# Kernel tuning notes

Hardware: AMD Instinct MI355X
Metric: run time of the kernel (lower is better)

The kernel has to match this reference:

```python
import jax, jax.numpy as jnp
import numpy as np

N, K, H, X_DIM, S_DIM = 50000, 8, 128, 32, 27
LSTM_IN = X_DIM + 3 * H  # 416


def setup_inputs() -> dict:
    key = jax.random.key(0)
    ks = jax.random.split(key, 16)

    def u(k, shape, fan_in):
        lim = 1.0 / np.sqrt(fan_in)
        return jax.random.uniform(k, shape, jnp.float32, -lim, lim)

    return {
        "x": jax.random.normal(ks[0], (N, X_DIM), jnp.float32),
        "h_self": jax.random.normal(ks[1], (N, H), jnp.float32),
        "c_self": jax.random.normal(ks[2], (N, H), jnp.float32),
        "h_inflows": jax.random.normal(ks[3], (N, K, H), jnp.float32),
        "inflow_valid": jax.random.randint(ks[4], (N, K), 0, 2) > 0,
        "static": jax.random.normal(ks[5], (N, S_DIM), jnp.float32),
        # Linear weights stored (out, in) as in eqx.nn.Linear
        "Wn": u(ks[6], (H, H), H),                     # W_neighbor, no bias
        "Wg": u(ks[7], (H, 2 * H), 2 * H),             # W_inflow_gate
        "bg": u(ks[8], (H,), 2 * H),
        "Ws": u(ks[9], (H, S_DIM), S_DIM),             # W_static
        "bs": u(ks[10], (H,), S_DIM),
        "Wl": u(ks[11], (4 * H, LSTM_IN), LSTM_IN),    # W_lstm
        "bl": u(ks[12], (4 * H,), LSTM_IN),
        "ln_w": jnp.ones((H,), jnp.float32),           # ln_h affine
        "ln_b": jnp.zeros((H,), jnp.float32),
    }


def reference(x, h_self, c_self, h_inflows, inflow_valid, static,
              Wn, Wg, bg, Ws, bs, Wl, bl, ln_w, ln_b):
    eps = 1e-5
    # per-neighbor message: [N,K,H]
    msgs = jnp.einsum('nkh,oh->nko', h_inflows, Wn)
    # inflow gate on concat(h_inflow, h_self): [N,K,H]
    h_tiled = jnp.broadcast_to(h_self[:, None, :], h_inflows.shape)
    gate_in = jnp.concatenate([h_inflows, h_tiled], axis=-1)  # [N,K,2H]
    gates = jax.nn.sigmoid(jnp.einsum('nkd,od->nko', gate_in, Wg) + bg)
    # masked sum over neighbors -> [N,H]
    mask = inflow_valid[..., None].astype(jnp.float32)
    neighbor_context = jnp.sum(gates * msgs * mask, axis=1)
    static_proj = static @ Ws.T + bs  # [N,H]
    combined = jnp.concatenate([x, h_self, neighbor_context, static_proj], axis=-1)
    z = combined @ Wl.T + bl  # [N,4H]
    i, f, o, g = jnp.split(z, 4, axis=-1)
    c_new = jax.nn.sigmoid(f) * c_self + jax.nn.sigmoid(i) * jnp.tanh(g)
    h_new = jax.nn.sigmoid(o) * jnp.tanh(c_new)
    # LayerNorm over hidden dim (eqx default eps=1e-5, affine)
    mu = jnp.mean(h_new, axis=-1, keepdims=True)
    var = jnp.mean(jnp.square(h_new - mu), axis=-1, keepdims=True)
    h_new = (h_new - mu) * jax.lax.rsqrt(var + eps) * ln_w + ln_b
    return (h_new, c_new)
```

## Files before the change

### kernel.cpp

```cpp
#include <hip/hip_runtime.h>
#include <hip/hip_bf16.h>

#define NN 50000
#define KI 8
#define H 128
#define XD 32
#define SD 27
#define CIN 416
#define CIN2 320
#define CPAD 328
#define ZOUT 512
#define NTILE_NB (NN / KI)
#define MB_LSTM 32

typedef __attribute__((ext_vector_type(8))) short bf16x8;
typedef __attribute__((ext_vector_type(4))) float f32x4;
typedef __attribute__((ext_vector_type(4))) unsigned short us4;

#define MFMA16(a, b, c) __builtin_amdgcn_mfma_f32_16x16x32_bf16((a), (b), (c), 0, 0, 0)

static __device__ __forceinline__ float sigmoidf_(float x) {
    return 1.0f / (1.0f + __expf(-x));
}
static __device__ __forceinline__ float tanhf_(float x) {
    return 1.0f - 2.0f / (__expf(2.0f * x) + 1.0f);
}
static __device__ __forceinline__ unsigned short bf(float f) {
    __hip_bfloat16 h = __float2bfloat16(f);
    return __builtin_bit_cast(unsigned short, h);
}
static __device__ __forceinline__ float dot4_(float4 a, float4 b) {
    return a.x * b.x + a.y * b.y + a.z * b.z + a.w * b.w;
}

__global__ __launch_bounds__(256) void k_prep(
    const float* __restrict__ Wn, const float* __restrict__ Wg,
    const float* __restrict__ Wl, const float* __restrict__ bl,
    const float* __restrict__ Ws, const float* __restrict__ bs,
    unsigned short* __restrict__ WnB, unsigned short* __restrict__ WgB,
    unsigned short* __restrict__ WpB, float* __restrict__ bp)
{
    const int b = blockIdx.x, t = threadIdx.x;
    if (b < 512) {
        const float* wr = Wl + (size_t)b * CIN;
        unsigned short* out = WpB + (size_t)b * CIN2;
        for (int c = t; c < CIN2; c += 256) {
            float v;
            if (c < 288) v = wr[c];
            else if (c < 288 + SD) {
                int s = c - 288;
                float acc = 0.f;
                for (int j = 0; j < H; ++j) acc += wr[288 + j] * Ws[j * SD + s];
                v = acc;
            } else v = 0.f;
            out[c] = bf(v);
        }
        if (t == 0) {
            float acc = bl[b];
            for (int j = 0; j < H; ++j) acc += wr[288 + j] * bs[j];
            bp[b] = acc;
        }
    } else {
        int idx = (b - 512) * 256 + t;
        for (int r = idx; r < 49152; r += 16384) {
            if (r < 16384) WnB[r] = bf(Wn[r]);
            else WgB[r - 16384] = bf(Wg[r - 16384]);
        }
    }
}

__global__ __launch_bounds__(256, 2) void k_nb_mfma(
    const float* __restrict__ hself_g, const float* __restrict__ hin_g,
    const unsigned char* __restrict__ valid_raw,
    const unsigned short* __restrict__ WnB, const unsigned short* __restrict__ WgB,
    const float* __restrict__ bg,
    unsigned short* __restrict__ ncb, int nc_stride)
{
    __shared__ unsigned short hin_s[64 * 128];
    __shared__ unsigned short hs_s[8 * 128];
    __shared__ float gh_s[8][128];
    __shared__ unsigned short ncs[8 * 128];
    __shared__ float valid_s[64];

    const int t = threadIdx.x;
    const int w = t >> 6, l = t & 63;
    const int ln = l & 15, lk = l >> 4;

    int det = 0;
    #pragma unroll
    for (int i = 0; i < 64; ++i) det |= valid_raw[4 * i + 1];
    const bool f8 = (det != 0);

    bf16x8 Bn[2][4], Ba[2][4], Bb[2][4];
    const int cbase = w * 32;
    #pragma unroll
    for (int c = 0; c < 2; ++c) {
        const int col = cbase + c * 16 + ln;
        #pragma unroll
        for (int kk = 0; kk < 4; ++kk) {
            const int k0 = kk * 32 + lk * 8;
            Bn[c][kk] = *(const bf16x8*)(WnB + col * H + k0);
            Ba[c][kk] = *(const bf16x8*)(WgB + col * 2 * H + k0);
            Bb[c][kk] = *(const bf16x8*)(WgB + col * 2 * H + H + k0);
        }
    }
    const float bg0 = bg[cbase + ln];
    const float bg1 = bg[cbase + 16 + ln];

    float4 ph[8], ps;
    float pv = 0.f;
    {
        const int nb0 = blockIdx.x * 8;
        const float4* src = (const float4*)(hin_g + (size_t)nb0 * KI * H);
        #pragma unroll
        for (int i = 0; i < 8; ++i) ph[i] = src[t + i * 256];
        ps = ((const float4*)(hself_g + (size_t)nb0 * H))[t];
        if (t < 64)
            pv = (f8 ? (valid_raw[(size_t)nb0 * KI + t] != 0)
                     : (((const unsigned int*)valid_raw)[(size_t)nb0 * KI + t] != 0u))
                     ? 1.f : 0.f;
    }

    for (int tile = blockIdx.x; tile < NTILE_NB; tile += gridDim.x) {
        const int nb = tile * 8;

        if (t < 64) valid_s[t] = pv;
        #pragma unroll
        for (int i = 0; i < 8; ++i) {
            int e = (t + i * 256) * 4, row = e >> 7, col = e & 127;
            unsigned byte = (unsigned)(row * 256 + col * 2) ^ (unsigned)((row & 7) << 4);
            us4 pk = { bf(ph[i].x), bf(ph[i].y), bf(ph[i].z), bf(ph[i].w) };
            *(us4*)((char*)hin_s + byte) = pk;
        }
        {
            int e = t * 4, row = e >> 7, col = e & 127;
            unsigned byte = (unsigned)(row * 256 + col * 2) ^ (unsigned)((row & 7) << 4);
            us4 pk = { bf(ps.x), bf(ps.y), bf(ps.z), bf(ps.w) };
            *(us4*)((char*)hs_s + byte) = pk;
        }
        __syncthreads();

        const int next = tile + gridDim.x;
        if (next < NTILE_NB) {
            const int nb2 = next * 8;
            const float4* src = (const float4*)(hin_g + (size_t)nb2 * KI * H);
            #pragma unroll
            for (int i = 0; i < 8; ++i) ph[i] = src[t + i * 256];
            ps = ((const float4*)(hself_g + (size_t)nb2 * H))[t];
            if (t < 64)
                pv = (f8 ? (valid_raw[(size_t)nb2 * KI + t] != 0)
                         : (((const unsigned int*)valid_raw)[(size_t)nb2 * KI + t] != 0u))
                         ? 1.f : 0.f;
        }

        f32x4 accM[4][2], accP[4][2], accG[2];
        #pragma unroll
        for (int m = 0; m < 4; ++m)
            #pragma unroll
            for (int c = 0; c < 2; ++c) { accM[m][c] = (f32x4)0.f; accP[m][c] = (f32x4)0.f; }
        accG[0] = (f32x4)0.f; accG[1] = (f32x4)0.f;

        #pragma unroll
        for (int kk = 0; kk < 4; ++kk) {
            const int k0 = kk * 32 + lk * 8;
            bf16x8 am[4];
            #pragma unroll
            for (int m = 0; m < 4; ++m) {
                int row = m * 16 + ln;
                unsigned byte = (unsigned)(row * 256 + k0 * 2) ^ (unsigned)((row & 7) << 4);
                am[m] = *(const bf16x8*)((const char*)hin_s + byte);
            }
            bf16x8 ah;
            {
                int row = ln & 7;
                unsigned byte = (unsigned)(row * 256 + k0 * 2) ^ (unsigned)((row & 7) << 4);
                ah = *(const bf16x8*)((const char*)hs_s + byte);
            }
            #pragma unroll
            for (int m = 0; m < 4; ++m)
                #pragma unroll
                for (int c = 0; c < 2; ++c) {
                    accM[m][c] = MFMA16(am[m], Bn[c][kk], accM[m][c]);
                    accP[m][c] = MFMA16(am[m], Ba[c][kk], accP[m][c]);
                }
            accG[0] = MFMA16(ah, Bb[0][kk], accG[0]);
            accG[1] = MFMA16(ah, Bb[1][kk], accG[1]);
        }

        #pragma unroll
        for (int c = 0; c < 2; ++c)
            #pragma unroll
            for (int r = 0; r < 4; ++r) {
                int row = lk * 4 + r;
                if (row < 8) gh_s[row][cbase + c * 16 + ln] = accG[c][r];
            }
        __syncthreads();

        #pragma unroll
        for (int m = 0; m < 4; ++m) {
            const int node = 2 * m + (lk >> 1);
            #pragma unroll
            for (int c = 0; c < 2; ++c) {
                const int col = cbase + c * 16 + ln;
                const float bgc = c ? bg1 : bg0;
                const float ghv = gh_s[node][col];
                float sum = 0.f;
                #pragma unroll
                for (int r = 0; r < 4; ++r) {
                    int row = m * 16 + lk * 4 + r;
                    float g = sigmoidf_(accP[m][c][r] + ghv + bgc);
                    sum += valid_s[row] * g * accM[m][c][r];
                }
                sum += __shfl_xor(sum, 16);
                if ((l & 16) == 0) ncs[(2 * m + (l >> 5)) * H + col] = bf(sum);
            }
        }
        __syncthreads();

        {
            int e = t * 4, node = e >> 7, col = e & 127;
            us4 v = *(const us4*)(ncs + e);
            *(us4*)(ncb + (size_t)(nb + node) * nc_stride + col) = v;
        }
    }
}

__global__ __launch_bounds__(512, 4) void k_lstm_mfma(
    const float* __restrict__ x_g, const float* __restrict__ hself_g,
    const float* __restrict__ cself_g, const float* __restrict__ stat_g,
    const unsigned short* __restrict__ ncb, int nc_stride,
    const unsigned short* __restrict__ WpB, const float* __restrict__ bp,
    const float* __restrict__ lnw, const float* __restrict__ lnb,
    float* __restrict__ h_out, float* __restrict__ c_out)
{
    __shared__ char smem[MB_LSTM * CPAD * 2];
    unsigned short* comb = (unsigned short*)smem;
    float (*hpre)[132] = (float(*)[132])smem;

    const int t = threadIdx.x;
    const int nb = blockIdx.x * MB_LSTM;
    const int w = t >> 6, l = t & 63, ln = l & 15, lk = l >> 4;
    const int hcol = w * 16 + ln;

    if (t < 256) {
        int e = t * 4, row = e >> 5, col = e & 31;
        us4 pk = { 0, 0, 0, 0 };
        if (nb + row < NN) {
            float4 v = ((const float4*)(x_g + (size_t)nb * XD))[t];
            pk = us4{ bf(v.x), bf(v.y), bf(v.z), bf(v.w) };
        }
        *(us4*)(comb + row * CPAD + col) = pk;
    }
    #pragma unroll
    for (int i = 0; i < 2; ++i) {
        int p4 = t + i * 512;
        int e = p4 * 4, row = e >> 7, col = 32 + (e & 127);
        us4 pk = { 0, 0, 0, 0 };
        if (nb + row < NN) {
            float4 v = ((const float4*)(hself_g + (size_t)nb * H))[p4];
            pk = us4{ bf(v.x), bf(v.y), bf(v.z), bf(v.w) };
        }
        *(us4*)(comb + row * CPAD + col) = pk;
    }
    #pragma unroll
    for (int i = 0; i < 2; ++i) {
        int p4 = t + i * 512;
        int e = p4 * 4, row = e >> 7, col = e & 127;
        us4 v = { 0, 0, 0, 0 };
        if (nb + row < NN) v = *(const us4*)(ncb + (size_t)(nb + row) * nc_stride + col);
        *(us4*)(comb + row * CPAD + 160 + col) = v;
    }
    for (int i = t; i < MB_LSTM * SD; i += 512) {
        int row = i / SD, col = i - row * SD;
        unsigned short v = 0;
        if (nb + row < NN) v = bf(stat_g[(size_t)(nb + row) * SD + col]);
        comb[row * CPAD + 288 + col] = v;
    }
    if (t < MB_LSTM * 5) {
        int row = t / 5, col = 315 + t % 5;
        comb[row * CPAD + col] = 0;
    }

    float cpre[8];
    #pragma unroll
    for (int m = 0; m < 2; ++m)
        #pragma unroll
        for (int r = 0; r < 4; ++r) {
            int node = m * 16 + lk * 4 + r;
            size_t n = (size_t)(nb + node);
            cpre[m * 4 + r] = (n < NN) ? cself_g[n * H + hcol] : 0.f;
        }
    __syncthreads();

    f32x4 acc[2][4];
    #pragma unroll
    for (int m = 0; m < 2; ++m)
        #pragma unroll
        for (int g = 0; g < 4; ++g) acc[m][g] = (f32x4)0.f;

    #pragma unroll
    for (int kk = 0; kk < 10; ++kk) {
        const int k0 = kk * 32 + lk * 8;
        bf16x8 a0 = *(const bf16x8*)(comb + ln * CPAD + k0);
        bf16x8 a1 = *(const bf16x8*)(comb + (16 + ln) * CPAD + k0);
        #pragma unroll
        for (int g = 0; g < 4; ++g) {
            bf16x8 b = *(const bf16x8*)(WpB + (size_t)(g * H + hcol) * CIN2 + k0);
            acc[0][g] = MFMA16(a0, b, acc[0][g]);
            acc[1][g] = MFMA16(a1, b, acc[1][g]);
        }
    }
    __syncthreads();

    {
        const float bi = bp[hcol], bff = bp[H + hcol];
        const float bo = bp[2 * H + hcol], bgg = bp[3 * H + hcol];
        #pragma unroll
        for (int m = 0; m < 2; ++m)
            #pragma unroll
            for (int r = 0; r < 4; ++r) {
                int node = m * 16 + lk * 4 + r;
                size_t n = (size_t)(nb + node);
                if (n < NN) {
                    float zi = acc[m][0][r] + bi;
                    float zf = acc[m][1][r] + bff;
                    float zo = acc[m][2][r] + bo;
                    float zg = acc[m][3][r] + bgg;
                    float cn = sigmoidf_(zf) * cpre[m * 4 + r] + sigmoidf_(zi) * tanhf_(zg);
                    c_out[n * H + hcol] = cn;
                    hpre[node][hcol] = sigmoidf_(zo) * tanhf_(cn);
                }
            }
    }
    __syncthreads();

    #pragma unroll
    for (int jj = 0; jj < 4; ++jj) {
        const int j = w * 4 + jj;
        const size_t n = (size_t)(nb + j);
        if (n < NN) {
            float a = hpre[j][l];
            float b = hpre[j][64 + l];
            float s = a + b, q = a * a + b * b;
            #pragma unroll
            for (int off = 1; off < 64; off <<= 1) {
                s += __shfl_xor(s, off);
                q += __shfl_xor(q, off);
            }
            float mu = s * (1.0f / 128.0f);
            float var = q * (1.0f / 128.0f) - mu * mu;
            float rstd = rsqrtf(var + 1e-5f);
            h_out[n * H + l]      = (a - mu) * rstd * lnw[l] + lnb[l];
            h_out[n * H + 64 + l] = (b - mu) * rstd * lnw[64 + l] + lnb[64 + l];
        }
    }
}

__global__ __launch_bounds__(256) void k_nb_f32(
    const float* __restrict__ hself_g, const float* __restrict__ hin_g,
    const unsigned char* __restrict__ valid_raw,
    const float* __restrict__ Wn, const float* __restrict__ Wg,
    const float* __restrict__ bg, float* __restrict__ nc)
{
    __shared__ float4 hin_s[8 * KI * (H / 4)];
    __shared__ float4 hs_s[8 * (H / 4)];
    __shared__ int flag8;
    const int t = threadIdx.x;
    const int nb = blockIdx.x * 8;
    {
        int loc = 0;
        if (t < 64) {
            #pragma unroll
            for (int i = 0; i < 16; ++i) loc |= valid_raw[4 * (t * 16 + i) + 1];
        }
        int any = __any(loc != 0);
        if (t == 0) flag8 = any;
    }
    const float4* src_hin = (const float4*)(hin_g + (size_t)nb * KI * H);
    #pragma unroll
    for (int i = 0; i < 8; ++i) hin_s[t + i * 256] = src_hin[t + i * 256];
    hs_s[t] = ((const float4*)(hself_g + (size_t)nb * H))[t];
    __syncthreads();
    const int o = t & 127, g = t >> 7;
    float msg[4][KI], gat[4][KI], gh[4];
    #pragma unroll
    for (int j = 0; j < 4; ++j) {
        gh[j] = 0.f;
        #pragma unroll
        for (int k = 0; k < KI; ++k) { msg[j][k] = 0.f; gat[j][k] = 0.f; }
    }
    const float4* Wn4 = (const float4*)(Wn + (size_t)o * H);
    const float4* Wg4a = (const float4*)(Wg + (size_t)o * 2 * H);
    const float4* Wg4b = (const float4*)(Wg + (size_t)o * 2 * H + H);
    for (int d4 = 0; d4 < H / 4; ++d4) {
        float4 wn = Wn4[d4], w0 = Wg4a[d4], w1 = Wg4b[d4];
        #pragma unroll
        for (int j = 0; j < 4; ++j) {
            const int node = g * 4 + j;
            gh[j] += dot4_(w1, hs_s[node * 32 + d4]);
            #pragma unroll
            for (int k = 0; k < KI; ++k) {
                float4 hv = hin_s[(node * KI + k) * 32 + d4];
                msg[j][k] += dot4_(wn, hv);
                gat[j][k] += dot4_(w0, hv);
            }
        }
    }
    const float bgo = bg[o];
    const unsigned int* valid32 = (const unsigned int*)valid_raw;
    const int f8 = flag8;
    #pragma unroll
    for (int j = 0; j < 4; ++j) {
        const int n = nb + g * 4 + j;
        float acc = 0.f;
        #pragma unroll
        for (int k = 0; k < KI; ++k) {
            bool v = f8 ? (valid_raw[n * KI + k] != 0) : (valid32[n * KI + k] != 0u);
            if (v) acc += sigmoidf_(gat[j][k] + gh[j] + bgo) * msg[j][k];
        }
        nc[(size_t)n * H + o] = acc;
    }
}

__global__ __launch_bounds__(256) void k_lstm_f32(
    const float* __restrict__ x_g, const float* __restrict__ hself_g,
    const float* __restrict__ cself_g, const float* __restrict__ stat_g,
    const float* __restrict__ nc,
    const float* __restrict__ Ws, const float* __restrict__ bs,
    const float* __restrict__ Wl, const float* __restrict__ bl,
    const float* __restrict__ lnw, const float* __restrict__ lnb,
    float* __restrict__ h_out, float* __restrict__ c_out)
{
    __shared__ float4 comb4[16 * (CIN / 4)];
    __shared__ float zsh[16 * ZOUT];
    __shared__ float stat_s[16 * SD];
    float* combf = (float*)comb4;
    const int t = threadIdx.x;
    const int nb = blockIdx.x * 16;
    #pragma unroll
    for (int i = 0; i < 2; ++i) {
        int idx = t + i * 256;
        combf[(idx >> 5) * CIN + (idx & 31)] = x_g[(size_t)nb * XD + idx];
    }
    #pragma unroll
    for (int i = 0; i < 8; ++i) {
        int idx = t + i * 256;
        combf[(idx >> 7) * CIN + 32 + (idx & 127)] = hself_g[(size_t)nb * H + idx];
    }
    #pragma unroll
    for (int i = 0; i < 8; ++i) {
        int idx = t + i * 256;
        combf[(idx >> 7) * CIN + 160 + (idx & 127)] = nc[(size_t)nb * H + idx];
    }
    stat_s[t] = stat_g[(size_t)nb * SD + t];
    if (t < 16 * SD - 256) stat_s[t + 256] = stat_g[(size_t)nb * SD + t + 256];
    __syncthreads();
    {
        const int o = t & 127, jg = t >> 7;
        #pragma unroll
        for (int jj = 0; jj < 8; ++jj) {
            const int j = jg * 8 + jj;
            float s = bs[o];
            #pragma unroll
            for (int c = 0; c < SD; ++c) s += Ws[o * SD + c] * stat_s[j * SD + c];
            combf[j * CIN + 288 + o] = s;
        }
    }
    __syncthreads();
    float acc0[16], acc1[16];
    #pragma unroll
    for (int j = 0; j < 16; ++j) { acc0[j] = 0.f; acc1[j] = 0.f; }
    const float4* W0 = (const float4*)(Wl + (size_t)t * CIN);
    const float4* W1 = (const float4*)(Wl + (size_t)(t + 256) * CIN);
    for (int d4 = 0; d4 < CIN / 4; ++d4) {
        float4 w0 = W0[d4], w1 = W1[d4];
        #pragma unroll
        for (int j = 0; j < 16; ++j) {
            float4 cv = comb4[j * (CIN / 4) + d4];
            acc0[j] += dot4_(w0, cv);
            acc1[j] += dot4_(w1, cv);
        }
    }
    const float bl0 = bl[t], bl1 = bl[t + 256];
    #pragma unroll
    for (int j = 0; j < 16; ++j) {
        zsh[j * ZOUT + t] = acc0[j] + bl0;
        zsh[j * ZOUT + 256 + t] = acc1[j] + bl1;
    }
    __syncthreads();
    {
        const int h = t & 127, jg = t >> 7;
        #pragma unroll
        for (int jj = 0; jj < 8; ++jj) {
            const int j = jg * 8 + jj;
            const size_t n = (size_t)(nb + j);
            float zi = zsh[j * ZOUT + h];
            float zf = zsh[j * ZOUT + 128 + h];
            float zo = zsh[j * ZOUT + 256 + h];
            float zg = zsh[j * ZOUT + 384 + h];
            float cn = sigmoidf_(zf) * cself_g[n * H + h] + sigmoidf_(zi) * tanhf(zg);
            c_out[n * H + h] = cn;
            zsh[j * ZOUT + h] = sigmoidf_(zo) * tanhf(cn);
        }
    }
    __syncthreads();
    {
        const int w = t >> 6, lane = t & 63;
        #pragma unroll
        for (int jj = 0; jj < 4; ++jj) {
            const int j = w * 4 + jj;
            const size_t n = (size_t)(nb + j);
            float a = zsh[j * ZOUT + lane];
            float b = zsh[j * ZOUT + 64 + lane];
            float s = a + b, q = a * a + b * b;
            #pragma unroll
            for (int off = 1; off < 64; off <<= 1) {
                s += __shfl_xor(s, off);
                q += __shfl_xor(q, off);
            }
            float mu = s * (1.0f / 128.0f);
            float var = q * (1.0f / 128.0f) - mu * mu;
            float rstd = rsqrtf(var + 1e-5f);
            h_out[n * H + lane] = (a - mu) * rstd * lnw[lane] + lnb[lane];
            h_out[n * H + 64 + lane] = (b - mu) * rstd * lnw[64 + lane] + lnb[64 + lane];
        }
    }
}

extern "C" void kernel_launch(void* const* d_in, const int* in_sizes, int n_in,
                              void* d_out, int out_size, void* d_ws, size_t ws_size,
                              hipStream_t stream) {
    const float* x      = (const float*)d_in[0];
    const float* h_self = (const float*)d_in[1];
    const float* c_self = (const float*)d_in[2];
    const float* h_inf  = (const float*)d_in[3];
    const unsigned char* valid = (const unsigned char*)d_in[4];
    const float* statp  = (const float*)d_in[5];
    const float* Wn     = (const float*)d_in[6];
    const float* Wg     = (const float*)d_in[7];
    const float* bg     = (const float*)d_in[8];
    const float* Ws     = (const float*)d_in[9];
    const float* bs     = (const float*)d_in[10];
    const float* Wl     = (const float*)d_in[11];
    const float* bl     = (const float*)d_in[12];
    const float* lnw    = (const float*)d_in[13];
    const float* lnb    = (const float*)d_in[14];

    float* h_out = (float*)d_out;
    float* c_out = h_out + (size_t)NN * H;

    const size_t W_BYTES = (size_t)512 * CIN2 * 2 + 16384 * 2 + 32768 * 2 + 512 * 4;
    const size_t NC_BYTES = (size_t)NN * H * 2;

    if (ws_size >= W_BYTES) {
        char* p = (char*)d_ws;
        unsigned short* WpB = (unsigned short*)p;           p += (size_t)512 * CIN2 * 2;
        unsigned short* WnB = (unsigned short*)p;           p += 16384 * 2;
        unsigned short* WgB = (unsigned short*)p;           p += 32768 * 2;
        float* bp = (float*)p;                              p += 512 * 4;

        unsigned short* ncb;
        int nc_stride;
        if (ws_size >= W_BYTES + NC_BYTES + 64) {
            ncb = (unsigned short*)p;
            nc_stride = H;
        } else {
            ncb = (unsigned short*)h_out;
            nc_stride = 256;
        }

        k_prep<<<576, 256, 0, stream>>>(Wn, Wg, Wl, bl, Ws, bs,
                                        WnB, WgB, WpB, bp);
        k_nb_mfma<<<512, 256, 0, stream>>>(h_self, h_inf, valid, WnB, WgB, bg,
                                           ncb, nc_stride);
        k_lstm_mfma<<<(NN + MB_LSTM - 1) / MB_LSTM, 512, 0, stream>>>(
            x, h_self, c_self, statp, ncb, nc_stride, WpB, bp,
            lnw, lnb, h_out, c_out);
    } else {
        float* nc_buf = (ws_size >= (size_t)NN * H * sizeof(float))
                            ? (float*)d_ws : h_out;
        k_nb_f32<<<NN / 8, 256, 0, stream>>>(h_self, h_inf, valid, Wn, Wg, bg, nc_buf);
        k_lstm_f32<<<NN / 16, 256, 0, stream>>>(x, h_self, c_self, statp, nc_buf,
                                                Ws, bs, Wl, bl, lnw, lnb, h_out, c_out);
    }
}
```

Baseline: 212.7 us.

## Cut register pressure in neighbor kernel to raise occupancy and grid size

The neighbor-message kernel no longer keeps all Wn/Wg B-fragments in registers or software-prefetches the next tile. Instead it reloads weight fragments from global/L2 inside the k-loop and processes the 64 neighbor rows in two halves, which shrinks the accumulator footprint. Launch bounds rise to 3 blocks per SM and the grid doubles to 1024 blocks, so more waves are resident to hide latency in place of explicit prefetching. The cost is repeated weight loads per tile and losing the register-level overlap of the next tile's global load with compute.

```diff
diff --git a/kernel.cpp b/kernel.cpp
--- a/kernel.cpp
+++ b/kernel.cpp
@@ -12,6 +12,7 @@
 #define ZOUT 512
 #define NTILE_NB (NN / KI)
 #define MB_LSTM 32
+#define GRID_NB 1024
 
 typedef __attribute__((ext_vector_type(8))) short bf16x8;
 typedef __attribute__((ext_vector_type(4))) float f32x4;
@@ -69,7 +70,7 @@
     }
 }
 
-__global__ __launch_bounds__(256, 2) void k_nb_mfma(
+__global__ __launch_bounds__(256, 3) void k_nb_mfma(
     const float* __restrict__ hself_g, const float* __restrict__ hin_g,
     const unsigned char* __restrict__ valid_raw,
     const unsigned short* __restrict__ WnB, const unsigned short* __restrict__ WgB,
@@ -91,100 +92,77 @@
     for (int i = 0; i < 64; ++i) det |= valid_raw[4 * i + 1];
     const bool f8 = (det != 0);
 
-    bf16x8 Bn[2][4], Ba[2][4], Bb[2][4];
     const int cbase = w * 32;
-    #pragma unroll
-    for (int c = 0; c < 2; ++c) {
-        const int col = cbase + c * 16 + ln;
+    const float bg0 = bg[cbase + ln];
+    const float bg1 = bg[cbase + 16 + ln];
+
+    for (int tile = blockIdx.x; tile < NTILE_NB; tile += gridDim.x) {
+        const int nb = tile * 8;
+
+        if (t < 64)
+            valid_s[t] = (f8 ? (valid_raw[(size_t)nb * KI + t] != 0)
+                             : (((const unsigned int*)valid_raw)[(size_t)nb * KI + t] != 0u))
+                             ? 1.f : 0.f;
+        {
+            const float4* src = (const float4*)(hin_g + (size_t)nb * KI * H);
+            float4 r0[8];
+            #pragma unroll
+            for (int i = 0; i < 8; ++i) r0[i] = src[t + i * 256];
+            float4 hv = ((const float4*)(hself_g + (size_t)nb * H))[t];
+            #pragma unroll
+            for (int i = 0; i < 8; ++i) {
+                int e = (t + i * 256) * 4, row = e >> 7, col = e & 127;
+                unsigned byte = (unsigned)(row * 256 + col * 2) ^ (unsigned)((row & 7) << 4);
+                us4 pk = { bf(r0[i].x), bf(r0[i].y), bf(r0[i].z), bf(r0[i].w) };
+                *(us4*)((char*)hin_s + byte) = pk;
+            }
+            {
+                int e = t * 4, row = e >> 7, col = e & 127;
+                unsigned byte = (unsigned)(row * 256 + col * 2) ^ (unsigned)((row & 7) << 4);
+                us4 pk = { bf(hv.x), bf(hv.y), bf(hv.z), bf(hv.w) };
+                *(us4*)((char*)hs_s + byte) = pk;
+            }
+        }
+        __syncthreads();
+
+        f32x4 aM[2][2], aP[2][2], aG[2];
+        #pragma unroll
+        for (int mm = 0; mm < 2; ++mm)
+            #pragma unroll
+            for (int c = 0; c < 2; ++c) { aM[mm][c] = (f32x4)0.f; aP[mm][c] = (f32x4)0.f; }
+        aG[0] = (f32x4)0.f; aG[1] = (f32x4)0.f;
+
         #pragma unroll
         for (int kk = 0; kk < 4; ++kk) {
             const int k0 = kk * 32 + lk * 8;
-            Bn[c][kk] = *(const bf16x8*)(WnB + col * H + k0);
-            Ba[c][kk] = *(const bf16x8*)(WgB + col * 2 * H + k0);
-            Bb[c][kk] = *(const bf16x8*)(WgB + col * 2 * H + H + k0);
-        }
-    }
-    const float bg0 = bg[cbase + ln];
-    const float bg1 = bg[cbase + 16 + ln];
-
-    float4 ph[8], ps;
-    float pv = 0.f;
-    {
-        const int nb0 = blockIdx.x * 8;
-        const float4* src = (const float4*)(hin_g + (size_t)nb0 * KI * H);
-        #pragma unroll
-        for (int i = 0; i < 8; ++i) ph[i] = src[t + i * 256];
-        ps = ((const float4*)(hself_g + (size_t)nb0 * H))[t];
-        if (t < 64)
-            pv = (f8 ? (valid_raw[(size_t)nb0 * KI + t] != 0)
-                     : (((const unsigned int*)valid_raw)[(size_t)nb0 * KI + t] != 0u))
-                     ? 1.f : 0.f;
-    }
-
-    for (int tile = blockIdx.x; tile < NTILE_NB; tile += gridDim.x) {
-        const int nb = tile * 8;
-
-        if (t < 64) valid_s[t] = pv;
-        #pragma unroll
-        for (int i = 0; i < 8; ++i) {
-            int e = (t + i * 256) * 4, row = e >> 7, col = e & 127;
-            unsigned byte = (unsigned)(row * 256 + col * 2) ^ (unsigned)((row & 7) << 4);
-            us4 pk = { bf(ph[i].x), bf(ph[i].y), bf(ph[i].z), bf(ph[i].w) };
-            *(us4*)((char*)hin_s + byte) = pk;
-        }
-        {
-            int e = t * 4, row = e >> 7, col = e & 127;
-            unsigned byte = (unsigned)(row * 256 + col * 2) ^ (unsigned)((row & 7) << 4);
-            us4 pk = { bf(ps.x), bf(ps.y), bf(ps.z), bf(ps.w) };
-            *(us4*)((char*)hs_s + byte) = pk;
-        }
-        __syncthreads();
-
-        const int next = tile + gridDim.x;
-        if (next < NTILE_NB) {
-            const int nb2 = next * 8;
-            const float4* src = (const float4*)(hin_g + (size_t)nb2 * KI * H);
-            #pragma unroll
-            for (int i = 0; i < 8; ++i) ph[i] = src[t + i * 256];
-            ps = ((const float4*)(hself_g + (size_t)nb2 * H))[t];
-            if (t < 64)
-                pv = (f8 ? (valid_raw[(size_t)nb2 * KI + t] != 0)
-                         : (((const unsigned int*)valid_raw)[(size_t)nb2 * KI + t] != 0u))
-                         ? 1.f : 0.f;
-        }
-
-        f32x4 accM[4][2], accP[4][2], accG[2];
-        #pragma unroll
-        for (int m = 0; m < 4; ++m)
-            #pragma unroll
-            for (int c = 0; c < 2; ++c) { accM[m][c] = (f32x4)0.f; accP[m][c] = (f32x4)0.f; }
-        accG[0] = (f32x4)0.f; accG[1] = (f32x4)0.f;
-
-        #pragma unroll
-        for (int kk = 0; kk < 4; ++kk) {
-            const int k0 = kk * 32 + lk * 8;
-            bf16x8 am[4];
-            #pragma unroll
-            for (int m = 0; m < 4; ++m) {
-                int row = m * 16 + ln;
+            bf16x8 am0, am1, ah;
+            {
+                int row = ln;
                 unsigned byte = (unsigned)(row * 256 + k0 * 2) ^ (unsigned)((row & 7) << 4);
-                am[m] = *(const bf16x8*)((const char*)hin_s + byte);
-            }
-            bf16x8 ah;
+                am0 = *(const bf16x8*)((const char*)hin_s + byte);
+            }
+            {
+                int row = 16 + ln;
+                unsigned byte = (unsigned)(row * 256 + k0 * 2) ^ (unsigned)((row & 7) << 4);
+                am1 = *(const bf16x8*)((const char*)hin_s + byte);
+            }
             {
                 int row = ln & 7;
                 unsigned byte = (unsigned)(row * 256 + k0 * 2) ^ (unsigned)((row & 7) << 4);
                 ah = *(const bf16x8*)((const char*)hs_s + byte);
             }
             #pragma unroll
-            for (int m = 0; m < 4; ++m)
-                #pragma unroll
-                for (int c = 0; c < 2; ++c) {
-                    accM[m][c] = MFMA16(am[m], Bn[c][kk], accM[m][c]);
-                    accP[m][c] = MFMA16(am[m], Ba[c][kk], accP[m][c]);
-                }
-            accG[0] = MFMA16(ah, Bb[0][kk], accG[0]);
-            accG[1] = MFMA16(ah, Bb[1][kk], accG[1]);
+            for (int c = 0; c < 2; ++c) {
+                const int col = cbase + c * 16 + ln;
+                bf16x8 bn = *(const bf16x8*)(WnB + col * H + k0);
+                bf16x8 ba = *(const bf16x8*)(WgB + col * 2 * H + k0);
+                bf16x8 bb = *(const bf16x8*)(WgB + col * 2 * H + H + k0);
+                aM[0][c] = MFMA16(am0, bn, aM[0][c]);
+                aM[1][c] = MFMA16(am1, bn, aM[1][c]);
+                aP[0][c] = MFMA16(am0, ba, aP[0][c]);
+                aP[1][c] = MFMA16(am1, ba, aP[1][c]);
+                aG[c]    = MFMA16(ah, bb, aG[c]);
+            }
         }
 
         #pragma unroll
@@ -192,13 +170,13 @@
             #pragma unroll
             for (int r = 0; r < 4; ++r) {
                 int row = lk * 4 + r;
-                if (row < 8) gh_s[row][cbase + c * 16 + ln] = accG[c][r];
+                if (row < 8) gh_s[row][cbase + c * 16 + ln] = aG[c][r];
             }
         __syncthreads();
 
         #pragma unroll
-        for (int m = 0; m < 4; ++m) {
-            const int node = 2 * m + (lk >> 1);
+        for (int mm = 0; mm < 2; ++mm) {
+            const int node = 2 * mm + (lk >> 1);
             #pragma unroll
             for (int c = 0; c < 2; ++c) {
                 const int col = cbase + c * 16 + ln;
@@ -207,12 +185,63 @@
                 float sum = 0.f;
                 #pragma unroll
                 for (int r = 0; r < 4; ++r) {
-                    int row = m * 16 + lk * 4 + r;
-                    float g = sigmoidf_(accP[m][c][r] + ghv + bgc);
-                    sum += valid_s[row] * g * accM[m][c][r];
+                    int row = mm * 16 + lk * 4 + r;
+                    float g = sigmoidf_(aP[mm][c][r] + ghv + bgc);
+                    sum += valid_s[row] * g * aM[mm][c][r];
                 }
                 sum += __shfl_xor(sum, 16);
-                if ((l & 16) == 0) ncs[(2 * m + (l >> 5)) * H + col] = bf(sum);
+                if ((l & 16) == 0) ncs[(2 * mm + (l >> 5)) * H + col] = bf(sum);
+            }
+        }
+
+        #pragma unroll
+        for (int mm = 0; mm < 2; ++mm)
+            #pragma unroll
+            for (int c = 0; c < 2; ++c) { aM[mm][c] = (f32x4)0.f; aP[mm][c] = (f32x4)0.f; }
+
+        #pragma unroll
+        for (int kk = 0; kk < 4; ++kk) {
+            const int k0 = kk * 32 + lk * 8;
+            bf16x8 am0, am1;
+            {
+                int row = 32 + ln;
+                unsigned byte = (unsigned)(row * 256 + k0 * 2) ^ (unsigned)((row & 7) << 4);
+                am0 = *(const bf16x8*)((const char*)hin_s + byte);
+            }
+            {
+                int row = 48 + ln;
+                unsigned byte = (unsigned)(row * 256 + k0 * 2) ^ (unsigned)((row & 7) << 4);
+                am1 = *(const bf16x8*)((const char*)hin_s + byte);
+            }
+            #pragma unroll
+            for (int c = 0; c < 2; ++c) {
+                const int col = cbase + c * 16 + ln;
+                bf16x8 bn = *(const bf16x8*)(WnB + col * H + k0);
+                bf16x8 ba = *(const bf16x8*)(WgB + col * 2 * H + k0);
+                aM[0][c] = MFMA16(am0, bn, aM[0][c]);
+                aM[1][c] = MFMA16(am1, bn, aM[1][c]);
+                aP[0][c] = MFMA16(am0, ba, aP[0][c]);
+                aP[1][c] = MFMA16(am1, ba, aP[1][c]);
+            }
+        }
+
+        #pragma unroll
+        for (int mm = 0; mm < 2; ++mm) {
+            const int node = 4 + 2 * mm + (lk >> 1);
+            #pragma unroll
+            for (int c = 0; c < 2; ++c) {
+                const int col = cbase + c * 16 + ln;
+                const float bgc = c ? bg1 : bg0;
+                const float ghv = gh_s[node][col];
+                float sum = 0.f;
+                #pragma unroll
+                for (int r = 0; r < 4; ++r) {
+                    int row = (2 + mm) * 16 + lk * 4 + r;
+                    float g = sigmoidf_(aP[mm][c][r] + ghv + bgc);
+                    sum += valid_s[row] * g * aM[mm][c][r];
+                }
+                sum += __shfl_xor(sum, 16);
+                if ((l & 16) == 0) ncs[(4 + 2 * mm + (l >> 5)) * H + col] = bf(sum);
             }
         }
         __syncthreads();
@@ -571,8 +600,8 @@
 
         k_prep<<<576, 256, 0, stream>>>(Wn, Wg, Wl, bl, Ws, bs,
                                         WnB, WgB, WpB, bp);
-        k_nb_mfma<<<512, 256, 0, stream>>>(h_self, h_inf, valid, WnB, WgB, bg,
-                                           ncb, nc_stride);
+        k_nb_mfma<<<GRID_NB, 256, 0, stream>>>(h_self, h_inf, valid, WnB, WgB, bg,
+                                               ncb, nc_stride);
         k_lstm_mfma<<<(NN + MB_LSTM - 1) / MB_LSTM, 512, 0, stream>>>(
             x, h_self, c_self, statp, ncb, nc_stride, WpB, bp,
             lnw, lnb, h_out, c_out);
```

After: 247.0 us. +16.1%, slower.

## Stream neighbor tiles via async global-to-LDS double buffering in k_nb_mfma

Applied to the files above, without the earlier changes.

The neighbor kernel now copies raw fp32 h_inflows and h_self tiles straight into LDS with global_load_lds into a double buffer, replacing the register prefetch and bf16 staging. The bf16 conversion moves to the fragment-load step. Weight fragments are reloaded from global/L2 on every k-step instead of being held in registers, which frees VGPRs. The valid mask is read directly into registers, and outputs are written straight to global, dropping two LDS staging buffers and one barrier. The cost is twice the LDS footprint, which may limit occupancy, plus repeated weight reads and conversion work inside the inner loop.

```diff
diff --git a/kernel.cpp b/kernel.cpp
--- a/kernel.cpp
+++ b/kernel.cpp
@@ -12,12 +12,17 @@
 #define ZOUT 512
 #define NTILE_NB (NN / KI)
 #define MB_LSTM 32
+#define GRID_NB 512
 
 typedef __attribute__((ext_vector_type(8))) short bf16x8;
 typedef __attribute__((ext_vector_type(4))) float f32x4;
 typedef __attribute__((ext_vector_type(4))) unsigned short us4;
+typedef __attribute__((ext_vector_type(8))) unsigned short us8;
 
 #define MFMA16(a, b, c) __builtin_amdgcn_mfma_f32_16x16x32_bf16((a), (b), (c), 0, 0, 0)
+
+typedef __attribute__((address_space(1))) const unsigned int gu32;
+typedef __attribute__((address_space(3))) unsigned int lu32;
 
 static __device__ __forceinline__ float sigmoidf_(float x) {
     return 1.0f / (1.0f + __expf(-x));
@@ -76,129 +81,139 @@
     const float* __restrict__ bg,
     unsigned short* __restrict__ ncb, int nc_stride)
 {
-    __shared__ unsigned short hin_s[64 * 128];
-    __shared__ unsigned short hs_s[8 * 128];
+    __shared__ __align__(16) float hinf[2][64 * 128];
+    __shared__ __align__(16) float hsf[2][8 * 128];
     __shared__ float gh_s[8][128];
-    __shared__ unsigned short ncs[8 * 128];
-    __shared__ float valid_s[64];
 
     const int t = threadIdx.x;
     const int w = t >> 6, l = t & 63;
     const int ln = l & 15, lk = l >> 4;
+    const int wb = __builtin_amdgcn_readfirstlane(w);
 
     int det = 0;
     #pragma unroll
     for (int i = 0; i < 64; ++i) det |= valid_raw[4 * i + 1];
     const bool f8 = (det != 0);
 
-    bf16x8 Bn[2][4], Ba[2][4], Bb[2][4];
     const int cbase = w * 32;
-    #pragma unroll
-    for (int c = 0; c < 2; ++c) {
-        const int col = cbase + c * 16 + ln;
+    const float bg0 = bg[cbase + ln];
+    const float bg1 = bg[cbase + 16 + ln];
+
+    int hin_off[8];
+    #pragma unroll
+    for (int i = 0; i < 8; ++i) {
+        int D = ((i * 4 + w) * 64 + l) * 16;
+        int row = D >> 9;
+        int inner = (D & 511) ^ ((row & 7) << 4);
+        hin_off[i] = row * 128 + (inner >> 2);
+    }
+    int hs_off;
+    {
+        int D = (w * 64 + l) * 16;
+        int row = D >> 9;
+        int inner = (D & 511) ^ ((row & 7) << 4);
+        hs_off = row * 128 + (inner >> 2);
+    }
+
+    {
+        const float* hb = hin_g + (size_t)blockIdx.x * 8 * KI * H;
+        #pragma unroll
+        for (int i = 0; i < 8; ++i)
+            __builtin_amdgcn_global_load_lds((gu32*)(hb + hin_off[i]),
+                (lu32*)&hinf[0][(i * 4 + wb) * 256], 16, 0, 0);
+        __builtin_amdgcn_global_load_lds(
+            (gu32*)(hself_g + (size_t)blockIdx.x * 8 * H + hs_off),
+            (lu32*)&hsf[0][wb * 256], 16, 0, 0);
+    }
+    __syncthreads();
+
+    int cur = 0;
+    for (int tile = blockIdx.x; tile < NTILE_NB; tile += GRID_NB) {
+        const int nb = tile * 8;
+
+        const int next = tile + GRID_NB;
+        if (next < NTILE_NB) {
+            const float* hb = hin_g + (size_t)next * 8 * KI * H;
+            #pragma unroll
+            for (int i = 0; i < 8; ++i)
+                __builtin_amdgcn_global_load_lds((gu32*)(hb + hin_off[i]),
+                    (lu32*)&hinf[cur ^ 1][(i * 4 + wb) * 256], 16, 0, 0);
+            __builtin_amdgcn_global_load_lds(
+                (gu32*)(hself_g + (size_t)next * 8 * H + hs_off),
+                (lu32*)&hsf[cur ^ 1][wb * 256], 16, 0, 0);
+        }
+
+        uint4 rv[4];
+        if (f8) {
+            const unsigned* vb = (const unsigned*)(valid_raw + (size_t)nb * KI);
+            #pragma unroll
+            for (int m = 0; m < 4; ++m) rv[m].x = vb[lk + 4 * m];
+        } else {
+            const uint4* vb = (const uint4*)((const unsigned*)valid_raw + (size_t)nb * KI);
+            #pragma unroll
+            for (int m = 0; m < 4; ++m) rv[m] = vb[lk + 4 * m];
+        }
+
+        const float* hbuf = hinf[cur];
+        const float* sbuf = hsf[cur];
+
+        f32x4 aM[4][2], aP[4][2], aG[2];
+        #pragma unroll
+        for (int m = 0; m < 4; ++m)
+            #pragma unroll
+            for (int c = 0; c < 2; ++c) { aM[m][c] = (f32x4)0.f; aP[m][c] = (f32x4)0.f; }
+        aG[0] = (f32x4)0.f; aG[1] = (f32x4)0.f;
+
         #pragma unroll
         for (int kk = 0; kk < 4; ++kk) {
             const int k0 = kk * 32 + lk * 8;
-            Bn[c][kk] = *(const bf16x8*)(WnB + col * H + k0);
-            Ba[c][kk] = *(const bf16x8*)(WgB + col * 2 * H + k0);
-            Bb[c][kk] = *(const bf16x8*)(WgB + col * 2 * H + H + k0);
-        }
-    }
-    const float bg0 = bg[cbase + ln];
-    const float bg1 = bg[cbase + 16 + ln];
-
-    float4 ph[8], ps;
-    float pv = 0.f;
-    {
-        const int nb0 = blockIdx.x * 8;
-        const float4* src = (const float4*)(hin_g + (size_t)nb0 * KI * H);
-        #pragma unroll
-        for (int i = 0; i < 8; ++i) ph[i] = src[t + i * 256];
-        ps = ((const float4*)(hself_g + (size_t)nb0 * H))[t];
-        if (t < 64)
-            pv = (f8 ? (valid_raw[(size_t)nb0 * KI + t] != 0)
-                     : (((const unsigned int*)valid_raw)[(size_t)nb0 * KI + t] != 0u))
-                     ? 1.f : 0.f;
-    }
-
-    for (int tile = blockIdx.x; tile < NTILE_NB; tile += gridDim.x) {
-        const int nb = tile * 8;
-
-        if (t < 64) valid_s[t] = pv;
-        #pragma unroll
-        for (int i = 0; i < 8; ++i) {
-            int e = (t + i * 256) * 4, row = e >> 7, col = e & 127;
-            unsigned byte = (unsigned)(row * 256 + col * 2) ^ (unsigned)((row & 7) << 4);
-            us4 pk = { bf(ph[i].x), bf(ph[i].y), bf(ph[i].z), bf(ph[i].w) };
-            *(us4*)((char*)hin_s + byte) = pk;
-        }
-        {
-            int e = t * 4, row = e >> 7, col = e & 127;
-            unsigned byte = (unsigned)(row * 256 + col * 2) ^ (unsigned)((row & 7) << 4);
-            us4 pk = { bf(ps.x), bf(ps.y), bf(ps.z), bf(ps.w) };
-            *(us4*)((char*)hs_s + byte) = pk;
-        }
-        __syncthreads();
-
-        const int next = tile + gridDim.x;
-        if (next < NTILE_NB) {
-            const int nb2 = next * 8;
-            const float4* src = (const float4*)(hin_g + (size_t)nb2 * KI * H);
-            #pragma unroll
-            for (int i = 0; i < 8; ++i) ph[i] = src[t + i * 256];
-            ps = ((const float4*)(hself_g + (size_t)nb2 * H))[t];
-            if (t < 64)
-                pv = (f8 ? (valid_raw[(size_t)nb2 * KI + t] != 0)
-                         : (((const unsigned int*)valid_raw)[(size_t)nb2 * KI + t] != 0u))
-                         ? 1.f : 0.f;
-        }
-
-        f32x4 accM[4][2], accP[4][2], accG[2];
-        #pragma unroll
-        for (int m = 0; m < 4; ++m)
-            #pragma unroll
-            for (int c = 0; c < 2; ++c) { accM[m][c] = (f32x4)0.f; accP[m][c] = (f32x4)0.f; }
-        accG[0] = (f32x4)0.f; accG[1] = (f32x4)0.f;
-
-        #pragma unroll
-        for (int kk = 0; kk < 4; ++kk) {
-            const int k0 = kk * 32 + lk * 8;
-            bf16x8 am[4];
+            bf16x8 am[4], ah;
             #pragma unroll
             for (int m = 0; m < 4; ++m) {
-                int row = m * 16 + ln;
-                unsigned byte = (unsigned)(row * 256 + k0 * 2) ^ (unsigned)((row & 7) << 4);
-                am[m] = *(const bf16x8*)((const char*)hin_s + byte);
-            }
-            bf16x8 ah;
+                const int row = m * 16 + ln;
+                const unsigned x = (unsigned)((row & 7) << 4);
+                const float4 q0 = *(const float4*)((const char*)hbuf + row * 512 + ((k0 * 4) ^ x));
+                const float4 q1 = *(const float4*)((const char*)hbuf + row * 512 + ((k0 * 4 + 16) ^ x));
+                us8 pk = { bf(q0.x), bf(q0.y), bf(q0.z), bf(q0.w),
+                           bf(q1.x), bf(q1.y), bf(q1.z), bf(q1.w) };
+                am[m] = __builtin_bit_cast(bf16x8, pk);
+            }
             {
-                int row = ln & 7;
-                unsigned byte = (unsigned)(row * 256 + k0 * 2) ^ (unsigned)((row & 7) << 4);
-                ah = *(const bf16x8*)((const char*)hs_s + byte);
-            }
-            #pragma unroll
-            for (int m = 0; m < 4; ++m)
+                const int row = ln & 7;
+                const unsigned x = (unsigned)(row << 4);
+                const float4 q0 = *(const float4*)((const char*)sbuf + row * 512 + ((k0 * 4) ^ x));
+                const float4 q1 = *(const float4*)((const char*)sbuf + row * 512 + ((k0 * 4 + 16) ^ x));
+                us8 pk = { bf(q0.x), bf(q0.y), bf(q0.z), bf(q0.w),
+                           bf(q1.x), bf(q1.y), bf(q1.z), bf(q1.w) };
+                ah = __builtin_bit_cast(bf16x8, pk);
+            }
+            #pragma unroll
+            for (int c = 0; c < 2; ++c) {
+                const int col = cbase + c * 16 + ln;
+                const bf16x8 bn = *(const bf16x8*)(WnB + col * H + k0);
+                const bf16x8 ba = *(const bf16x8*)(WgB + col * 2 * H + k0);
+                const bf16x8 bb = *(const bf16x8*)(WgB + col * 2 * H + H + k0);
                 #pragma unroll
-                for (int c = 0; c < 2; ++c) {
-                    accM[m][c] = MFMA16(am[m], Bn[c][kk], accM[m][c]);
-                    accP[m][c] = MFMA16(am[m], Ba[c][kk], accP[m][c]);
+                for (int m = 0; m < 4; ++m) {
+                    aM[m][c] = MFMA16(am[m], bn, aM[m][c]);
+                    aP[m][c] = MFMA16(am[m], ba, aP[m][c]);
                 }
-            accG[0] = MFMA16(ah, Bb[0][kk], accG[0]);
-            accG[1] = MFMA16(ah, Bb[1][kk], accG[1]);
+                aG[c] = MFMA16(ah, bb, aG[c]);
+            }
         }
 
         #pragma unroll
         for (int c = 0; c < 2; ++c)
             #pragma unroll
             for (int r = 0; r < 4; ++r) {
-                int row = lk * 4 + r;
-                if (row < 8) gh_s[row][cbase + c * 16 + ln] = accG[c][r];
-            }
-        __syncthreads();
+                const int row = lk * 4 + r;
+                if (row < 8) gh_s[row][cbase + c * 16 + ln] = aG[c][r];
+            }
 
         #pragma unroll
         for (int m = 0; m < 4; ++m) {
             const int node = 2 * m + (lk >> 1);
+            const uint4 rvm = rv[m];
             #pragma unroll
             for (int c = 0; c < 2; ++c) {
                 const int col = cbase + c * 16 + ln;
@@ -207,21 +222,23 @@
                 float sum = 0.f;
                 #pragma unroll
                 for (int r = 0; r < 4; ++r) {
-                    int row = m * 16 + lk * 4 + r;
-                    float g = sigmoidf_(accP[m][c][r] + ghv + bgc);
-                    sum += valid_s[row] * g * accM[m][c][r];
+                    const unsigned uw = (r == 0) ? rvm.x : (r == 1) ? rvm.y
+                                      : (r == 2) ? rvm.z : rvm.w;
+                    const bool vf = f8 ? (((rvm.x >> (8 * r)) & 0xffu) != 0u)
+                                       : (uw != 0u);
+                    const float g = sigmoidf_(aP[m][c][r] + ghv + bgc);
+                    sum += vf ? g * aM[m][c][r] : 0.f;
                 }
                 sum += __shfl_xor(sum, 16);
-                if ((l & 16) == 0) ncs[(2 * m + (l >> 5)) * H + col] = bf(sum);
-            }
-        }
+                if ((l & 16) == 0) {
+                    const int node_o = 2 * m + (l >> 5);
+                    ncb[(size_t)(nb + node_o) * nc_stride + col] = bf(sum);
+                }
+            }
+        }
+
         __syncthreads();
-
-        {
-            int e = t * 4, node = e >> 7, col = e & 127;
-            us4 v = *(const us4*)(ncs + e);
-            *(us4*)(ncb + (size_t)(nb + node) * nc_stride + col) = v;
-        }
+        cur ^= 1;
     }
 }
 
@@ -571,8 +588,8 @@
 
         k_prep<<<576, 256, 0, stream>>>(Wn, Wg, Wl, bl, Ws, bs,
                                         WnB, WgB, WpB, bp);
-        k_nb_mfma<<<512, 256, 0, stream>>>(h_self, h_inf, valid, WnB, WgB, bg,
-                                           ncb, nc_stride);
+        k_nb_mfma<<<GRID_NB, 256, 0, stream>>>(h_self, h_inf, valid, WnB, WgB, bg,
+                                               ncb, nc_stride);
         k_lstm_mfma<<<(NN + MB_LSTM - 1) / MB_LSTM, 512, 0, stream>>>(
             x, h_self, c_self, statp, ncb, nc_stride, WpB, bp,
             lnw, lnb, h_out, c_out);
```

Measured after the change: 245.9 us. 1.16x slower.
